# Performance work log

Measured on AMD Instinct MI355X. Metric: run time of the kernel, lower is better.

The kernel has to match this reference:

```python
import jax, jax.numpy as jnp
import numpy as np

HEADS = 4
SPARSITY_WEIGHT = 0.1
LN_EPS = 1e-5


def setup_inputs() -> dict:
    key = jax.random.key(0)
    ks = jax.random.split(key, 6)
    b, n, d = 4, 2048, 512
    x = jax.random.normal(ks[0], (b, n, d), dtype=jnp.float32)
    alibi_bias = jax.random.normal(ks[1], (b, n, n), dtype=jnp.float32)
    gamma = jax.random.normal(ks[2], (b, d), dtype=jnp.float32)
    beta = jax.random.normal(ks[3], (b, d), dtype=jnp.float32)
    ln_w = jnp.ones((d,), dtype=jnp.float32)
    ln_b = jnp.zeros((d,), dtype=jnp.float32)
    w_qkv = jax.random.normal(ks[4], (d, 3 * d), dtype=jnp.float32) * (d ** -0.5)
    w_out = jax.random.normal(ks[5], (d, d), dtype=jnp.float32) * (d ** -0.5)
    return {"x": x, "alibi_bias": alibi_bias, "gamma": gamma, "beta": beta,
            "ln_w": ln_w, "ln_b": ln_b, "w_qkv": w_qkv, "w_out": w_out}


def reference(x, alibi_bias, gamma, beta, ln_w, ln_b, w_qkv, w_out):
    b, n, d = x.shape
    dh = d // HEADS
    scale = dh ** -0.5
    # LayerNorm over last dim
    mu = jnp.mean(x, axis=-1, keepdims=True)
    var = jnp.mean(jnp.square(x - mu), axis=-1, keepdims=True)
    xn = (x - mu) * jax.lax.rsqrt(var + LN_EPS) * ln_w + ln_b
    # FiLM
    xn = gamma[:, None, :] * xn + beta[:, None, :]
    # QKV projection (Linear, no bias)
    qkv = xn @ w_qkv  # [b, n, 3d]
    q, k, v = jnp.split(qkv, 3, axis=-1)
    split_heads = lambda t: t.reshape(b, n, HEADS, dh).transpose(0, 2, 1, 3)  # b h n d
    q, k, v = split_heads(q), split_heads(k), split_heads(v)
    dots = jnp.einsum('bhid,bhjd->bhij', q, k) * scale
    dots = dots + alibi_bias[:, None, :, :]  # broadcast over heads
    attn = jax.nn.softmax(dots, axis=-1)
    eps = 1e-8
    entropy = -(attn * jnp.log(attn + eps)).sum(axis=-1)
    sparsity_loss = entropy.mean() * SPARSITY_WEIGHT
    out = jnp.einsum('bhij,bhjd->bhid', attn, v)
    out = out.transpose(0, 2, 1, 3).reshape(b, n, d)
    return out @ w_out, sparsity_loss
```

## Files before the change

### kernel.cpp

```cpp
#include <hip/hip_runtime.h>
#include <hip/hip_bf16.h>

typedef __attribute__((ext_vector_type(8))) short short8;
typedef __attribute__((ext_vector_type(4))) short short4_t;
typedef __attribute__((ext_vector_type(4))) float f32x4;

static constexpr int NN = 2048, DD = 512;
static constexpr float SCALE = 0.088388347648318447f;
static constexpr float ENT_SCALE = 0.1f / 32768.0f;

__device__ __forceinline__ short f2bf(float f) {
  __hip_bfloat16 h = __float2bfloat16(f);
  return *reinterpret_cast<short*>(&h);
}

__device__ __forceinline__ void async_cp16(const void* g, void* l) {
  __builtin_amdgcn_global_load_lds((const __attribute__((address_space(1))) void*)g,
                                   (__attribute__((address_space(3))) void*)l, 16, 0, 0);
}

__global__ __launch_bounds__(256) void ln_film_k(
    const float* __restrict__ x, const float* __restrict__ gamma,
    const float* __restrict__ beta, const float* __restrict__ lnw,
    const float* __restrict__ lnb, short* __restrict__ xn) {
  const int wave = threadIdx.x >> 6, lane = threadIdx.x & 63;
  const int row = blockIdx.x * 4 + wave;
  const int b = row >> 11;
  const float4* xr = reinterpret_cast<const float4*>(x + (size_t)row * DD);
  float4 u = xr[lane * 2], v = xr[lane * 2 + 1];
  float s  = u.x + u.y + u.z + u.w + v.x + v.y + v.z + v.w;
  float ss = u.x*u.x + u.y*u.y + u.z*u.z + u.w*u.w + v.x*v.x + v.y*v.y + v.z*v.z + v.w*v.w;
  #pragma unroll
  for (int m = 1; m < 64; m <<= 1) { s += __shfl_xor(s, m); ss += __shfl_xor(ss, m); }
  const float mu = s * (1.0f / DD);
  const float rs = rsqrtf(ss * (1.0f / DD) - mu * mu + 1e-5f);
  const int c0 = lane * 8;
  float vals[8] = {u.x,u.y,u.z,u.w,v.x,v.y,v.z,v.w};
  short8 o;
  #pragma unroll
  for (int i = 0; i < 8; ++i) {
    const int c = c0 + i;
    const float t = (vals[i] - mu) * rs * lnw[c] + lnb[c];
    o[i] = f2bf(gamma[b * DD + c] * t + beta[b * DD + c]);
  }
  *reinterpret_cast<short8*>(xn + (size_t)row * DD + c0) = o;
}

__global__ void prep_w_k(const float* __restrict__ wqkv, const float* __restrict__ wout,
                         short* __restrict__ wqkvT, short* __restrict__ woutT) {
  int id = blockIdx.x * 256 + threadIdx.x;
  if (id < 786432) {
    const int k = id / 1536, c = id - k * 1536;
    wqkvT[(size_t)c * 512 + k] = f2bf(wqkv[id]);
  } else {
    id -= 786432;
    const int k = id >> 9, c = id & 511;
    woutT[(size_t)c * 512 + k] = f2bf(wout[id]);
  }
}

__global__ __launch_bounds__(256) void vt_k(const short* __restrict__ qkv, short* __restrict__ vt) {
  __shared__ short t[64][136];
  const int bh = blockIdx.y;
  const int b = bh >> 2, h = bh & 3;
  const int k0 = blockIdx.x * 64;
  const int tid = threadIdx.x;
  const int key = tid >> 2, part = tid & 3;
  const short* src = qkv + ((size_t)(b * NN + k0 + key) * 1536 + 1024 + h * 128 + part * 32);
  #pragma unroll
  for (int i = 0; i < 4; ++i) {
    short8 v = *reinterpret_cast<const short8*>(src + i * 8);
    #pragma unroll
    for (int j = 0; j < 8; ++j) t[key][part * 32 + i * 8 + j] = v[j];
  }
  __syncthreads();
  const int dh = tid >> 1, half = tid & 1;
  short* dst = vt + ((size_t)(bh * 128 + dh) * NN + k0 + half * 32);
  #pragma unroll
  for (int i = 0; i < 4; ++i) {
    short8 o;
    #pragma unroll
    for (int j = 0; j < 8; ++j) o[j] = t[half * 32 + i * 8 + j][dh];
    *reinterpret_cast<short8*>(dst + i * 8) = o;
  }
}

template<int BM, int NT, bool BF16OUT>
__global__ __launch_bounds__(256) void gemm_bt_k(
    const short* __restrict__ A, const short* __restrict__ Bt, void* __restrict__ C) {
  constexpr int K = 512;
  constexpr int ABYTES = BM * 128;
  __shared__ char lds[2 * ABYTES + 32768];
  constexpr int nTiles = NT / 128;
  const int m0 = (blockIdx.x / nTiles) * BM;
  const int n0 = (blockIdx.x % nTiles) * 128;
  const int tid = threadIdx.x, wave = tid >> 6, lane = tid & 63;
  const int wm = wave >> 1, wn = wave & 1;
  const int lg = lane >> 4, li = lane & 15;
  constexpr int MT = BM / 32;
  f32x4 acc[MT][4] = {};

  auto stage = [&](int buf, int kt) {
    #pragma unroll
    for (int t = 0; t < BM / 32; ++t) {
      const int dbase = t * 4096 + wave * 1024;
      const int m = (dbase >> 7) + (lane >> 3);
      const int cs = ((lane & 7) * 16) ^ ((m & 7) << 4);
      async_cp16((const char*)A + ((size_t)(m0 + m) * K + kt * 64) * 2 + cs,
                 lds + buf * ABYTES + dbase);
    }
    #pragma unroll
    for (int t = 0; t < 4; ++t) {
      const int dbase = t * 4096 + wave * 1024;
      const int n = (dbase >> 7) + (lane >> 3);
      const int cs = ((lane & 7) * 16) ^ ((n & 7) << 4);
      async_cp16((const char*)Bt + ((size_t)(n0 + n) * K + kt * 64) * 2 + cs,
                 lds + 2 * ABYTES + buf * 16384 + dbase);
    }
  };

  stage(0, 0);
  __syncthreads();
  for (int kt = 0; kt < 8; ++kt) {
    const int cur = kt & 1;
    if (kt < 7) stage(cur ^ 1, kt + 1);
    const char* Al = lds + cur * ABYTES;
    const char* Bl = lds + 2 * ABYTES + cur * 16384;
    #pragma unroll
    for (int ks = 0; ks < 2; ++ks) {
      const int kb = ks * 64 + lg * 16;
      short8 af[MT], bfr[4];
      #pragma unroll
      for (int t = 0; t < MT; ++t) {
        const int r = wm * (BM / 2) + t * 16 + li;
        af[t] = *reinterpret_cast<const short8*>(Al + r * 128 + (kb ^ ((r & 7) << 4)));
      }
      #pragma unroll
      for (int t = 0; t < 4; ++t) {
        const int c = wn * 64 + t * 16 + li;
        bfr[t] = *reinterpret_cast<const short8*>(Bl + c * 128 + (kb ^ ((c & 7) << 4)));
      }
      #pragma unroll
      for (int mt = 0; mt < MT; ++mt)
        #pragma unroll
        for (int nt = 0; nt < 4; ++nt)
          acc[mt][nt] = __builtin_amdgcn_mfma_f32_16x16x32_bf16(af[mt], bfr[nt], acc[mt][nt], 0, 0, 0);
    }
    __syncthreads();
  }
  #pragma unroll
  for (int mt = 0; mt < MT; ++mt) {
    #pragma unroll
    for (int nt = 0; nt < 4; ++nt) {
      const int row = m0 + wm * (BM / 2) + mt * 16 + lg * 4;
      const int col = n0 + wn * 64 + nt * 16 + li;
      #pragma unroll
      for (int r = 0; r < 4; ++r) {
        if (BF16OUT)
          reinterpret_cast<short*>(C)[(size_t)(row + r) * NT + col] = f2bf(acc[mt][nt][r]);
        else
          reinterpret_cast<float*>(C)[(size_t)(row + r) * NT + col] = acc[mt][nt][r];
      }
    }
  }
}

__global__ __launch_bounds__(256) void attn_k(
    const short* __restrict__ qkv, const short* __restrict__ vt,
    const float* __restrict__ alibi, short* __restrict__ ao, float* __restrict__ ent) {
  __shared__ char lds[73728];
  const int qt = blockIdx.x, bh = blockIdx.y;
  const int b = bh >> 2, h = bh & 3;
  const int tid = threadIdx.x, wave = tid >> 6, lane = tid & 63;
  const int lg = lane >> 4, li = lane & 15;
  char* const Pbase = lds + 65536 + wave * 2048;

  const int qrow = qt * 64 + wave * 16 + li;
  const char* qptr = (const char*)qkv + ((size_t)(b * NN + qrow) * 1536 + h * 128) * 2;
  short8 qf[4];
  #pragma unroll
  for (int kq = 0; kq < 4; ++kq)
    qf[kq] = *reinterpret_cast<const short8*>(qptr + kq * 64 + lg * 16);

  f32x4 oacc[8] = {};
  float mrow = -INFINITY, lrow = 0.f, trow = 0.f;
  const float* arow = alibi + (size_t)(b * NN + qrow) * NN;

  auto stageK = [&](int buf, int kt) {
    #pragma unroll
    for (int i = 0; i < 4; ++i) {
      const int chunk = wave * 4 + i;
      const int row = chunk * 4 + (lane >> 4);
      const int cs = ((lane & 15) * 16) ^ ((row & 15) << 4);
      async_cp16((const char*)qkv + ((size_t)(b * NN + kt * 64 + row) * 1536 + 512 + h * 128) * 2 + cs,
                 lds + buf * 16384 + chunk * 1024);
    }
  };
  auto stageV = [&](int buf, int kt) {
    #pragma unroll
    for (int i = 0; i < 4; ++i) {
      const int chunk = wave * 4 + i;
      const int row = chunk * 8 + (lane >> 3);
      const int cs = ((lane & 7) * 16) ^ ((row & 7) << 4);
      async_cp16((const char*)vt + ((size_t)(bh * 128 + row) * NN + kt * 64) * 2 + cs,
                 lds + 32768 + buf * 16384 + chunk * 1024);
    }
  };
  auto loadA = [&](int kt, float4* ab) {
    #pragma unroll
    for (int ct = 0; ct < 4; ++ct)
      ab[ct] = *reinterpret_cast<const float4*>(arow + kt * 64 + ct * 16 + lg * 4);
  };

  float4 abE[4], abO[4];
  stageK(0, 0); stageV(0, 0);
  loadA(0, abE); loadA(1, abO);
  __syncthreads();

  #pragma unroll 1
  for (int kt2 = 0; kt2 < 32; kt2 += 2) {
    #pragma unroll
    for (int par = 0; par < 2; ++par) {
      const int kt = kt2 + par;
      const int cur = par, nxt = par ^ 1;
      float4* const ab = par ? abO : abE;
      if (kt < 31) { stageK(nxt, kt + 1); stageV(nxt, kt + 1); }

      f32x4 sacc[4] = {};
      const char* Kl = lds + cur * 16384;
      #pragma unroll
      for (int ct = 0; ct < 4; ++ct) {
        const int key = ct * 16 + li;
        #pragma unroll
        for (int kq = 0; kq < 4; ++kq) {
          short8 kf = *reinterpret_cast<const short8*>(
              Kl + key * 256 + ((kq * 64 + lg * 16) ^ ((key & 15) << 4)));
          sacc[ct] = __builtin_amdgcn_mfma_f32_16x16x32_bf16(kf, qf[kq], sacc[ct], 0, 0, 0);
        }
      }
      float sv[4][4], p[4][4];
      #pragma unroll
      for (int ct = 0; ct < 4; ++ct) {
        sv[ct][0] = fmaf(sacc[ct][0], SCALE, ab[ct].x);
        sv[ct][1] = fmaf(sacc[ct][1], SCALE, ab[ct].y);
        sv[ct][2] = fmaf(sacc[ct][2], SCALE, ab[ct].z);
        sv[ct][3] = fmaf(sacc[ct][3], SCALE, ab[ct].w);
      }
      if (kt + 2 < 32) loadA(kt + 2, ab);

      float mx = sv[0][0];
      #pragma unroll
      for (int ct = 0; ct < 4; ++ct)
        #pragma unroll
        for (int r = 0; r < 4; ++r) mx = fmaxf(mx, sv[ct][r]);
      mx = fmaxf(mx, __shfl_xor(mx, 16));
      mx = fmaxf(mx, __shfl_xor(mx, 32));
      const bool resc = !__all(mx <= mrow + 8.0f);
      float newm = mrow, fsc = 1.0f;
      if (resc) { newm = fmaxf(mrow, mx); fsc = __expf(mrow - newm); }
      float lsum = 0.f, tsum = 0.f;
      #pragma unroll
      for (int ct = 0; ct < 4; ++ct)
        #pragma unroll
        for (int r = 0; r < 4; ++r) {
          p[ct][r] = __expf(sv[ct][r] - newm);
          lsum += p[ct][r];
          tsum = fmaf(p[ct][r], sv[ct][r], tsum);
        }
      lsum += __shfl_xor(lsum, 16); lsum += __shfl_xor(lsum, 32);
      tsum += __shfl_xor(tsum, 16); tsum += __shfl_xor(tsum, 32);
      if (resc) {
        lrow = lrow * fsc + lsum; trow = trow * fsc + tsum; mrow = newm;
        #pragma unroll
        for (int nt = 0; nt < 8; ++nt) oacc[nt] *= fsc;
      } else { lrow += lsum; trow += tsum; }

      #pragma unroll
      for (int ct = 0; ct < 4; ++ct) {
        short4_t pw;
        #pragma unroll
        for (int r = 0; r < 4; ++r) pw[r] = f2bf(p[ct][r]);
        *reinterpret_cast<short4_t*>(Pbase + li * 128 + ((ct * 32 + lg * 8) ^ ((li & 7) << 4))) = pw;
      }
      const char* Vl = lds + 32768 + cur * 16384;
      #pragma unroll
      for (int ks = 0; ks < 2; ++ks) {
        const int kb = ks * 64 + lg * 16;
        short8 pa = *reinterpret_cast<const short8*>(Pbase + li * 128 + (kb ^ ((li & 7) << 4)));
        #pragma unroll
        for (int nt = 0; nt < 8; ++nt) {
          const int dh = nt * 16 + li;
          short8 vb = *reinterpret_cast<const short8*>(Vl + dh * 128 + (kb ^ ((dh & 7) << 4)));
          oacc[nt] = __builtin_amdgcn_mfma_f32_16x16x32_bf16(vb, pa, oacc[nt], 0, 0, 0);
        }
      }
      __syncthreads();
    }
  }

  const float invl = 1.0f / lrow;
  #pragma unroll
  for (int nt = 0; nt < 8; ++nt) {
    short4_t ow;
    #pragma unroll
    for (int r = 0; r < 4; ++r) ow[r] = f2bf(oacc[nt][r] * invl);
    *reinterpret_cast<short4_t*>(ao + (size_t)(b * NN + qrow) * DD + h * 128 + nt * 16 + lg * 4) = ow;
  }
  float e = (lg == 0) ? (mrow + logf(lrow) - trow * invl) : 0.f;
  #pragma unroll
  for (int m = 1; m < 64; m <<= 1) e += __shfl_xor(e, m);
  if (lane == 0) atomicAdd(ent, e * ENT_SCALE);
}

extern "C" void kernel_launch(void* const* d_in, const int* in_sizes, int n_in,
                              void* d_out, int out_size, void* d_ws, size_t ws_size,
                              hipStream_t stream) {
  const float* x     = (const float*)d_in[0];
  const float* alibi = (const float*)d_in[1];
  const float* gamma = (const float*)d_in[2];
  const float* beta  = (const float*)d_in[3];
  const float* lnw   = (const float*)d_in[4];
  const float* lnb   = (const float*)d_in[5];
  const float* wqkv  = (const float*)d_in[6];
  const float* wout  = (const float*)d_in[7];
  float* out = (float*)d_out;

  char* ws = (char*)d_ws;
  short* xn    = (short*)(ws);
  short* wqkvT = (short*)(ws + 8388608);
  short* woutT = (short*)(ws + 9961472);
  short* qkv   = (short*)(ws + 10485760);
  short* vt    = (short*)(ws + 35651584);
  short* ao    = (short*)(ws);

  hipMemsetAsync(out + 4194304, 0, 4, stream);
  ln_film_k<<<2048, 256, 0, stream>>>(x, gamma, beta, lnw, lnb, xn);
  prep_w_k<<<4096, 256, 0, stream>>>(wqkv, wout, wqkvT, woutT);
  gemm_bt_k<64, 1536, true><<<128 * 12, 256, 0, stream>>>(xn, wqkvT, qkv);
  vt_k<<<dim3(32, 16), 256, 0, stream>>>(qkv, vt);
  attn_k<<<dim3(32, 16), 256, 0, stream>>>(qkv, vt, alibi, ao, out + 4194304);
  gemm_bt_k<64, 512, false><<<128 * 4, 256, 0, stream>>>(ao, woutT, out);
}
```

Measured before the change: 247.1 us.

## Overlap async loads via partial vmcnt waits, raise MFMA priority, retile QKV GEMM

Swaps the full __syncthreads after staging for explicit s_waitcnt vmcnt(N) plus s_barrier in both the GEMM and attention loops. The next tile's global-to-LDS copies can then stay in flight while the current tile is consumed, and s_setprio wraps the MFMA blocks. The weight-prep kernel is rewritten so each thread writes 16-byte vectors along the transposed dimension instead of scattered 2-byte stores. The QKV GEMM moves to BM=128 tiles. The hand-tuned vmcnt counts must exactly match the number of outstanding loads per stage, or the kernel reads stale LDS.

```diff
diff --git a/kernel.cpp b/kernel.cpp
--- a/kernel.cpp
+++ b/kernel.cpp
@@ -46,17 +46,22 @@
   *reinterpret_cast<short8*>(xn + (size_t)row * DD + c0) = o;
 }
 
-__global__ void prep_w_k(const float* __restrict__ wqkv, const float* __restrict__ wout,
-                         short* __restrict__ wqkvT, short* __restrict__ woutT) {
-  int id = blockIdx.x * 256 + threadIdx.x;
-  if (id < 786432) {
-    const int k = id / 1536, c = id - k * 1536;
-    wqkvT[(size_t)c * 512 + k] = f2bf(wqkv[id]);
-  } else {
-    id -= 786432;
-    const int k = id >> 9, c = id & 511;
-    woutT[(size_t)c * 512 + k] = f2bf(wout[id]);
-  }
+__global__ __launch_bounds__(256) void prep_w_k(
+    const float* __restrict__ wqkv, const float* __restrict__ wout,
+    short* __restrict__ wqkvT, short* __restrict__ woutT) {
+  const int id = blockIdx.x;
+  const float* src; short* dst; int C, k0, c0;
+  if (id < 192) { src = wqkv; dst = wqkvT; C = 1536; k0 = (id / 24) * 64; c0 = (id % 24) * 64; }
+  else { const int i2 = id - 192; src = wout; dst = woutT; C = 512; k0 = (i2 >> 3) * 64; c0 = (i2 & 7) * 64; }
+  const int c  = c0 + (threadIdx.x & 63);
+  const int kb = k0 + (threadIdx.x >> 6) * 16;
+  short8 o0, o1;
+  #pragma unroll
+  for (int j = 0; j < 8; ++j) o0[j] = f2bf(src[(size_t)(kb + j) * C + c]);
+  #pragma unroll
+  for (int j = 0; j < 8; ++j) o1[j] = f2bf(src[(size_t)(kb + 8 + j) * C + c]);
+  *reinterpret_cast<short8*>(dst + (size_t)c * 512 + kb)     = o0;
+  *reinterpret_cast<short8*>(dst + (size_t)c * 512 + kb + 8) = o1;
 }
 
 __global__ __launch_bounds__(256) void vt_k(const short* __restrict__ qkv, short* __restrict__ vt) {
@@ -120,10 +125,18 @@
   };
 
   stage(0, 0);
-  __syncthreads();
   for (int kt = 0; kt < 8; ++kt) {
     const int cur = kt & 1;
     if (kt < 7) stage(cur ^ 1, kt + 1);
+    __builtin_amdgcn_sched_barrier(0);
+    if (kt < 7) {
+      if constexpr (BM == 128) asm volatile("s_waitcnt vmcnt(8)" ::: "memory");
+      else                     asm volatile("s_waitcnt vmcnt(6)" ::: "memory");
+    } else {
+      asm volatile("s_waitcnt vmcnt(0)" ::: "memory");
+    }
+    __builtin_amdgcn_s_barrier();
+    __builtin_amdgcn_sched_barrier(0);
     const char* Al = lds + cur * ABYTES;
     const char* Bl = lds + 2 * ABYTES + cur * 16384;
     #pragma unroll
@@ -140,13 +153,16 @@
         const int c = wn * 64 + t * 16 + li;
         bfr[t] = *reinterpret_cast<const short8*>(Bl + c * 128 + (kb ^ ((c & 7) << 4)));
       }
+      __builtin_amdgcn_s_setprio(1);
       #pragma unroll
       for (int mt = 0; mt < MT; ++mt)
         #pragma unroll
         for (int nt = 0; nt < 4; ++nt)
           acc[mt][nt] = __builtin_amdgcn_mfma_f32_16x16x32_bf16(af[mt], bfr[nt], acc[mt][nt], 0, 0, 0);
-    }
-    __syncthreads();
+      __builtin_amdgcn_s_setprio(0);
+    }
+    __builtin_amdgcn_sched_barrier(0);
+    __builtin_amdgcn_s_barrier();
   }
   #pragma unroll
   for (int mt = 0; mt < MT; ++mt) {
@@ -215,7 +231,6 @@
   float4 abE[4], abO[4];
   stageK(0, 0); stageV(0, 0);
   loadA(0, abE); loadA(1, abO);
-  __syncthreads();
 
   #pragma unroll 1
   for (int kt2 = 0; kt2 < 32; kt2 += 2) {
@@ -225,9 +240,15 @@
       const int cur = par, nxt = par ^ 1;
       float4* const ab = par ? abO : abE;
       if (kt < 31) { stageK(nxt, kt + 1); stageV(nxt, kt + 1); }
+      __builtin_amdgcn_sched_barrier(0);
+      if (kt < 31) asm volatile("s_waitcnt vmcnt(12)" ::: "memory");
+      else         asm volatile("s_waitcnt vmcnt(0)"  ::: "memory");
+      __builtin_amdgcn_s_barrier();
+      __builtin_amdgcn_sched_barrier(0);
 
       f32x4 sacc[4] = {};
       const char* Kl = lds + cur * 16384;
+      __builtin_amdgcn_s_setprio(1);
       #pragma unroll
       for (int ct = 0; ct < 4; ++ct) {
         const int key = ct * 16 + li;
@@ -238,6 +259,8 @@
           sacc[ct] = __builtin_amdgcn_mfma_f32_16x16x32_bf16(kf, qf[kq], sacc[ct], 0, 0, 0);
         }
       }
+      __builtin_amdgcn_s_setprio(0);
+
       float sv[4][4], p[4][4];
       #pragma unroll
       for (int ct = 0; ct < 4; ++ct) {
@@ -283,6 +306,7 @@
         *reinterpret_cast<short4_t*>(Pbase + li * 128 + ((ct * 32 + lg * 8) ^ ((li & 7) << 4))) = pw;
       }
       const char* Vl = lds + 32768 + cur * 16384;
+      __builtin_amdgcn_s_setprio(1);
       #pragma unroll
       for (int ks = 0; ks < 2; ++ks) {
         const int kb = ks * 64 + lg * 16;
@@ -294,7 +318,9 @@
           oacc[nt] = __builtin_amdgcn_mfma_f32_16x16x32_bf16(vb, pa, oacc[nt], 0, 0, 0);
         }
       }
-      __syncthreads();
+      __builtin_amdgcn_s_setprio(0);
+      __builtin_amdgcn_sched_barrier(0);
+      __builtin_amdgcn_s_barrier();
     }
   }
 
@@ -335,8 +361,8 @@
 
   hipMemsetAsync(out + 4194304, 0, 4, stream);
   ln_film_k<<<2048, 256, 0, stream>>>(x, gamma, beta, lnw, lnb, xn);
-  prep_w_k<<<4096, 256, 0, stream>>>(wqkv, wout, wqkvT, woutT);
-  gemm_bt_k<64, 1536, true><<<128 * 12, 256, 0, stream>>>(xn, wqkvT, qkv);
+  prep_w_k<<<256, 256, 0, stream>>>(wqkv, wout, wqkvT, woutT);
+  gemm_bt_k<128, 1536, true><<<64 * 12, 256, 0, stream>>>(xn, wqkvT, qkv);
   vt_k<<<dim3(32, 16), 256, 0, stream>>>(qkv, vt);
   attn_k<<<dim3(32, 16), 256, 0, stream>>>(qkv, vt, alibi, ao, out + 4194304);
   gemm_bt_k<64, 512, false><<<128 * 4, 256, 0, stream>>>(ao, woutT, out);
```

Result: no change. 243.1 us (-1.6%).
